# Optimization experiments

Measured on AMD Instinct MI355X. Metric: run time of the kernel, lower is better.

## Reference

```python
import jax, jax.numpy as jnp
import numpy as np

B, L = 64, 200
NQ = 1024          # n_question == output_dim
NPID = 4096
D = 256            # q_embed_dim
H = 512            # hidden_dim
Q = 1024           # output_dim
L2 = 1e-05


def setup_inputs() -> dict:
    key = jax.random.key(0)
    ks = jax.random.split(key, 20)
    q_data = jax.random.randint(ks[0], (B, L), 1, NQ + 1)          # question ids in [1, NQ]
    ans = jax.random.randint(ks[1], (B, L), 0, 2)
    qa_data = q_data + NQ * ans                                     # encoded (q, answer)
    pid_data = jax.random.randint(ks[2], (B, L), 0, NPID + 1)
    matrix = jax.random.uniform(ks[3], (Q, Q), jnp.float32) * 0.05  # p_c_relations
    u = jax.random.uniform(ks[4], (B, L))
    target = jnp.where(u < 0.1, -1.0, jnp.where(u < 0.55, 0.0, 1.0)).astype(jnp.float32)
    s = 0.05
    q_emb = jax.random.normal(ks[5], (NQ + 1, D), jnp.float32) * s
    qa_emb = jax.random.normal(ks[6], (2, D), jnp.float32) * s
    q_emb_diff = jax.random.normal(ks[7], (NQ + 1, D), jnp.float32) * s
    qa_emb_diff = jax.random.normal(ks[8], (2 * NQ + 1, D), jnp.float32) * s
    diff_parm = jax.random.normal(ks[9], (NPID + 1, 1), jnp.float32) * s
    gs = 1.0 / np.sqrt(H).astype(np.float32)
    w_ih = jax.random.uniform(ks[10], (3 * H, 2 * D), jnp.float32, -gs, gs)
    w_hh = jax.random.uniform(ks[11], (3 * H, H), jnp.float32, -gs, gs)
    b_ih = jax.random.uniform(ks[12], (3 * H,), jnp.float32, -gs, gs)
    b_hh = jax.random.uniform(ks[13], (3 * H,), jnp.float32, -gs, gs)
    fc_w = jax.random.normal(ks[14], (Q, H), jnp.float32) * 0.02
    fc_b = jnp.zeros((Q,), jnp.float32)
    return dict(q_data=q_data, qa_data=qa_data, pid_data=pid_data, matrix=matrix,
                target=target, q_emb=q_emb, qa_emb=qa_emb, q_emb_diff=q_emb_diff,
                qa_emb_diff=qa_emb_diff, diff_parm=diff_parm, w_ih=w_ih, w_hh=w_hh,
                b_ih=b_ih, b_hh=b_hh, fc_w=fc_w, fc_b=fc_b)


def _gru(x, w_ih, w_hh, b_ih, b_hh):
    # PyTorch GRU, single layer, batch_first. x: [B, L, In]
    xg = jnp.einsum('bli,gi->blg', x, w_ih) + b_ih          # [B, L, 3H]
    def step(h, xg_t):
        hg = h @ w_hh.T + b_hh
        xr, xz, xn = jnp.split(xg_t, 3, axis=-1)
        hr, hz, hn = jnp.split(hg, 3, axis=-1)
        r = jax.nn.sigmoid(xr + hr)
        z = jax.nn.sigmoid(xz + hz)
        n = jnp.tanh(xn + r * hn)
        h_new = (1.0 - z) * n + z * h
        return h_new, h_new
    h0 = jnp.zeros((x.shape[0], w_hh.shape[1]), x.dtype)
    _, hs = jax.lax.scan(step, h0, xg.transpose(1, 0, 2))
    return hs.transpose(1, 0, 2)                             # [B, L, H]


def reference(q_data, qa_data, pid_data, matrix, target, q_emb, qa_emb,
              q_emb_diff, qa_emb_diff, diff_parm, w_ih, w_hh, b_ih, b_hh,
              fc_w, fc_b):
    q_embed = q_emb[q_data]                                  # [B, L, D]
    qa = (qa_data - q_data) // NQ                            # answer in {0,1}
    qa_embed = qa_emb[qa] + q_embed
    pid_embed = diff_parm[pid_data]                          # [B, L, 1]
    q_embed2 = q_embed + pid_embed * q_emb_diff[q_data]
    qa_embed2 = qa_embed + pid_embed * qa_emb_diff[qa]
    c_reg = (pid_embed ** 2).sum() * L2

    x = jnp.concatenate([qa_embed2, q_embed2], axis=-1)      # [B, L, 2D]
    gru_out = _gru(x, w_ih, w_hh, b_ih, b_hh)
    gru_out = jnp.einsum('blh,qh->blq', gru_out, fc_w) + fc_b  # [B, L, Q]

    got = jnp.einsum('blq,kq->blk', gru_out, matrix)         # [B, L, Q]
    master = jnp.where(got >= 0.4, 1.0, got)                 # threshold-to-1 only
    # mastery of the question asked at step t: master[b, t, q-1]
    mvals = jnp.take_along_axis(master, (q_data - 1)[..., None], axis=2)[..., 0]  # [B, L]

    f32 = jnp.float32
    eq = (q_data[:, :, None] == q_data[:, None, :]).astype(f32)   # [B, t, k]
    t_idx = jnp.arange(L)
    tri_strict = (t_idx[:, None] > t_idx[None, :]).astype(f32)    # k < t
    tri_incl = (t_idx[:, None] >= t_idx[None, :]).astype(f32)     # k <= t
    mast = (mvals == 1.0).astype(f32)
    notm = (mvals == 0.0).astype(f32)
    qa1 = (qa == 1).astype(f32)
    qa0 = 1.0 - qa1
    base = eq * tri_strict                                        # [B, L, L]
    mc = jnp.einsum('btk,bk->bt', base, qa1 * mast)   # master_correct
    mi = jnp.einsum('btk,bk->bt', base, qa0 * mast)   # master_incorrect
    nmc = jnp.einsum('btk,bk->bt', base, qa0 * notm)  # no_master_correct
    aa = jnp.einsum('btk,tk->bt', eq, tri_incl)       # answered_all (>= 1)

    arB = jnp.arange(B)
    idx = q_data - 1

    def dina_step(carry, xs):
        guess, slip = carry                            # [B, Q] each
        i_t, m_t, qa_t, mc_t, mi_t, nmc_t, aa_t = xs   # [B] each
        g_upd = jnp.where(m_t == 1.0, mc_t / aa_t,
                          jnp.where(qa_t == 0, 1.0 - nmc_t / aa_t, nmc_t / aa_t))
        upd_slip = (m_t == 1.0) & (qa_t == 0)
        new_g = jnp.where(upd_slip, guess[arB, i_t], g_upd)
        new_s = jnp.where(upd_slip, mi_t / aa_t, slip[arB, i_t])
        guess = guess.at[arB, i_t].set(new_g)
        slip = slip.at[arB, i_t].set(new_s)
        p = (1.0 - new_s) * (m_t * new_g + (1.0 - new_s) * (1.0 - m_t))
        return (guess, slip), p

    init = (jnp.zeros((B, Q), f32), jnp.zeros((B, Q), f32))
    xs = (idx.T, mvals.T, qa.T, mc.T, mi.T, nmc.T, aa.T)
    _, ps = jax.lax.scan(dina_step, init, xs)          # [L, B]
    preds = ps.T.reshape(-1)                           # [B*L]

    labels = target.reshape(-1)
    mask = labels > -0.9
    preds_d = jax.lax.stop_gradient(preds)             # torch detaches via torch.tensor()
    mse_sum = (((preds_d - labels) ** 2) * mask.astype(f32)).sum()
    loss = mse_sum + c_reg
    return (loss, jax.nn.sigmoid(preds_d), mask.sum())
```

## Files before the change

kernel.cpp:

```cpp
#include <hip/hip_runtime.h>
#include <hip/hip_bf16.h>
#include <math.h>

#define BB 64
#define LL 200
#define NQ 1024
#define DD 256
#define HH 512
#define QQ 1024
#define G3 1536
#define BL 12800
#define GBLK 256

#define OFF_ACC   ((size_t)0)
#define OFF_CELLS ((size_t)16)
#define OFF_HA    ((size_t)1056)
#define OFF_AQ    (OFF_HA + 65536)
#define OFF_DQ    (OFF_AQ + 1574400)
#define OFF_BQA   (OFF_DQ + 1574400)
#define OFF_CQA   (OFF_BQA + 3072)
#define OFF_WSUM  (OFF_CQA + 3072)
#define OFF_FCWT  (OFF_WSUM + 393216)
#define OFF_M2    (OFF_FCWT + 524288)
#define OFF_MB    (OFF_M2 + 524288)
#define OFF_XG    (OFF_MB + 1024)
#define OFF_GRUT  (OFF_XG + 19660800)
#define OFF_QINT  (OFF_GRUT + 6553600)
#define OFF_QAINT (OFF_QINT + 12800)
#define OFF_PIDF  (OFF_QAINT + 12800)
#define OFF_MVAL  (OFF_PIDF + 12800)
#define OFF_MC    (OFF_MVAL + 12800)
#define OFF_MI    (OFF_MC + 12800)
#define OFF_NMC   (OFF_MI + 12800)
#define OFF_AA    (OFF_NMC + 12800)
#define OFF_PREDS (OFF_AA + 12800)

typedef float f32x4 __attribute__((ext_vector_type(4)));

__device__ __forceinline__ float wave_sum64(float v) {
    #pragma unroll
    for (int o = 32; o > 0; o >>= 1) v += __shfl_down(v, o, 64);
    return v;
}

__device__ __forceinline__ f32x4 llc_load4(const float* p) {
    f32x4 v;
    asm volatile("global_load_dwordx4 %0, %1, off sc0 sc1" : "=v"(v) : "v"(p));
    return v;
}
__device__ __forceinline__ void llc_wait2(f32x4& a, f32x4& b) {
    asm volatile("s_waitcnt vmcnt(0)" : "+v"(a), "+v"(b));
}
__device__ __forceinline__ void llc_store1(float* p, float v) {
    asm volatile("global_store_dword %0, %1, off sc0 sc1" :: "v"(p), "v"(v) : "memory");
}

__device__ __forceinline__ float quad_sum(float v) {
    float t1 = __int_as_float(__builtin_amdgcn_update_dpp(
        0, __float_as_int(v), 0xB1, 0xF, 0xF, true));
    v += t1;
    float t2 = __int_as_float(__builtin_amdgcn_update_dpp(
        0, __float_as_int(v), 0x4E, 0xF, 0xF, true));
    return v + t2;
}

__global__ __launch_bounds__(256) void prep_meta(
    const int* __restrict__ q_data, const int* __restrict__ qa_data,
    const int* __restrict__ pid_data, const float* __restrict__ diff_parm,
    int* __restrict__ qint, int* __restrict__ qaint, float* __restrict__ pidf,
    float* __restrict__ acc)
{
    int r = blockIdx.x * 256 + threadIdx.x;
    float pp = 0.f;
    if (r < BL) {
        int q = q_data[r];
        qint[r] = q;
        qaint[r] = (qa_data[r] - q) / NQ;
        float pid = diff_parm[pid_data[r]];
        pidf[r] = pid;
        pp = pid * pid;
    }
    pp = wave_sum64(pp);
    __shared__ float sm[4];
    int lane = threadIdx.x & 63, w = threadIdx.x >> 6;
    if (lane == 0) sm[w] = pp;
    __syncthreads();
    if (threadIdx.x == 0) atomicAdd(&acc[0], sm[0] + sm[1] + sm[2] + sm[3]);
}

__global__ __launch_bounds__(256) void wsum_kernel(const float* __restrict__ w_ih,
                                                   float* __restrict__ wsum)
{
    int g = blockIdx.x, d = threadIdx.x;
    wsum[(size_t)g * DD + d] = w_ih[(size_t)g * 2 * DD + d] + w_ih[(size_t)g * 2 * DD + DD + d];
}

__global__ __launch_bounds__(256) void transpose_kernel(const float* __restrict__ in,
                                                        float* __restrict__ out, int R, int C)
{
    __shared__ float tile[32][33];
    int r0 = blockIdx.y * 32, c0 = blockIdx.x * 32;
    int tx = threadIdx.x & 31, ty = threadIdx.x >> 5;
    #pragma unroll
    for (int i = 0; i < 32; i += 8) {
        int r = r0 + ty + i, c = c0 + tx;
        if (r < R && c < C) tile[ty + i][tx] = in[(size_t)r * C + c];
    }
    __syncthreads();
    #pragma unroll
    for (int i = 0; i < 32; i += 8) {
        int c = c0 + ty + i, r = r0 + tx;
        if (c < C && r < R) out[(size_t)c * R + r] = tile[tx][ty + i];
    }
}

__global__ __launch_bounds__(256) void gemm_nt_dual(
    const float* __restrict__ A0, const float* __restrict__ A1, int lda,
    const float* __restrict__ B0, const float* __restrict__ B1, int ldb0, int ldb1,
    float* __restrict__ C0, float* __restrict__ C1, int ldc,
    int M, int N, int K,
    const float* __restrict__ bias0, const float* __restrict__ bias1)
{
    const int z = blockIdx.z;
    const float* A = z ? A1 : A0;
    const float* B = z ? B1 : B0;
    float* C = z ? C1 : C0;
    const int ldb = z ? ldb1 : ldb0;
    const float* bias = z ? bias1 : bias0;

    __shared__ float As[16][65];
    __shared__ float Bs[16][65];
    const int bm = blockIdx.y * 64, bn = blockIdx.x * 64;
    const int tid = threadIdx.x;
    const int tx = tid & 15, ty = tid >> 4;
    const int mm = tid >> 4, kk = tid & 15;
    float acc[4][4] = {};
    float ar[4], br[4];
    #pragma unroll
    for (int i = 0; i < 4; ++i) {
        int m = bm + mm + 16 * i;
        ar[i] = (m < M) ? A[(size_t)m * lda + kk] : 0.f;
        int n = bn + mm + 16 * i;
        br[i] = (n < N) ? B[(size_t)n * ldb + kk] : 0.f;
    }
    for (int k0 = 0; k0 < K; k0 += 16) {
        #pragma unroll
        for (int i = 0; i < 4; ++i) { As[kk][mm + 16 * i] = ar[i]; Bs[kk][mm + 16 * i] = br[i]; }
        __syncthreads();
        int kn = k0 + 16;
        if (kn < K) {
            #pragma unroll
            for (int i = 0; i < 4; ++i) {
                int m = bm + mm + 16 * i;
                ar[i] = (m < M) ? A[(size_t)m * lda + kn + kk] : 0.f;
                int n = bn + mm + 16 * i;
                br[i] = (n < N) ? B[(size_t)n * ldb + kn + kk] : 0.f;
            }
        }
        #pragma unroll
        for (int kq = 0; kq < 16; ++kq) {
            float a[4], b[4];
            #pragma unroll
            for (int i = 0; i < 4; ++i) a[i] = As[kq][ty * 4 + i];
            #pragma unroll
            for (int j = 0; j < 4; ++j) b[j] = Bs[kq][tx * 4 + j];
            #pragma unroll
            for (int i = 0; i < 4; ++i)
                #pragma unroll
                for (int j = 0; j < 4; ++j) acc[i][j] += a[i] * b[j];
        }
        __syncthreads();
    }
    #pragma unroll
    for (int i = 0; i < 4; ++i) {
        int m = bm + ty * 4 + i;
        if (m >= M) continue;
        #pragma unroll
        for (int j = 0; j < 4; ++j) {
            int n = bn + tx * 4 + j;
            if (n >= N) continue;
            C[(size_t)m * ldc + n] = acc[i][j] + (bias ? bias[n] : 0.f);
        }
    }
}

__global__ __launch_bounds__(256) void gemm_nt_splitk(
    const float* __restrict__ Ain, int lda,
    const float* __restrict__ Bin, int ldb,
    float* __restrict__ Cp, int ldc,
    int M, int N, int K4)
{
    const int z = blockIdx.z;
    const float* A = Ain + (size_t)z * K4;
    const float* B = Bin + (size_t)z * K4;
    float* C = Cp + (size_t)z * M * ldc;

    __shared__ float As[16][65];
    __shared__ float Bs[16][65];
    const int bm = blockIdx.y * 64, bn = blockIdx.x * 64;
    const int tid = threadIdx.x;
    const int tx = tid & 15, ty = tid >> 4;
    const int mm = tid >> 4, kk = tid & 15;
    float acc[4][4] = {};
    float ar[4], br[4];
    #pragma unroll
    for (int i = 0; i < 4; ++i) {
        int m = bm + mm + 16 * i;
        ar[i] = (m < M) ? A[(size_t)m * lda + kk] : 0.f;
        int n = bn + mm + 16 * i;
        br[i] = (n < N) ? B[(size_t)n * ldb + kk] : 0.f;
    }
    for (int k0 = 0; k0 < K4; k0 += 16) {
        #pragma unroll
        for (int i = 0; i < 4; ++i) { As[kk][mm + 16 * i] = ar[i]; Bs[kk][mm + 16 * i] = br[i]; }
        __syncthreads();
        int kn = k0 + 16;
        if (kn < K4) {
            #pragma unroll
            for (int i = 0; i < 4; ++i) {
                int m = bm + mm + 16 * i;
                ar[i] = (m < M) ? A[(size_t)m * lda + kn + kk] : 0.f;
                int n = bn + mm + 16 * i;
                br[i] = (n < N) ? B[(size_t)n * ldb + kn + kk] : 0.f;
            }
        }
        #pragma unroll
        for (int kq = 0; kq < 16; ++kq) {
            float a[4], b[4];
            #pragma unroll
            for (int i = 0; i < 4; ++i) a[i] = As[kq][ty * 4 + i];
            #pragma unroll
            for (int j = 0; j < 4; ++j) b[j] = Bs[kq][tx * 4 + j];
            #pragma unroll
            for (int i = 0; i < 4; ++i)
                #pragma unroll
                for (int j = 0; j < 4; ++j) acc[i][j] += a[i] * b[j];
        }
        __syncthreads();
    }
    #pragma unroll
    for (int i = 0; i < 4; ++i) {
        int m = bm + ty * 4 + i;
        if (m >= M) continue;
        #pragma unroll
        for (int j = 0; j < 4; ++j) {
            int n = bn + tx * 4 + j;
            if (n >= N) continue;
            C[(size_t)m * ldc + n] = acc[i][j];
        }
    }
}

__global__ __launch_bounds__(256) void reduce4_kernel(const float* __restrict__ p,
                                                      float* __restrict__ o, int n)
{
    int i = blockIdx.x * 256 + threadIdx.x;
    if (i < n) o[i] = p[i] + p[n + i] + p[2 * n + i] + p[3 * n + i];
}

__global__ __launch_bounds__(256) void mb_kernel(const float* __restrict__ matrix,
                                                 const float* __restrict__ fc_b,
                                                 float* __restrict__ mb)
{
    int k = blockIdx.x;
    float s = 0.f;
    for (int q = threadIdx.x; q < QQ; q += 256) s += matrix[(size_t)k * QQ + q] * fc_b[q];
    s = wave_sum64(s);
    __shared__ float sm[4];
    int lane = threadIdx.x & 63, w = threadIdx.x >> 6;
    if (lane == 0) sm[w] = s;
    __syncthreads();
    if (threadIdx.x == 0) mb[k] = sm[0] + sm[1] + sm[2] + sm[3];
}

__global__ __launch_bounds__(512) void xgt_kernel(
    const float* __restrict__ Aq, const float* __restrict__ Bqa,
    const float* __restrict__ Cqa, const float* __restrict__ Dq,
    const int* __restrict__ qint, const int* __restrict__ qaint,
    const float* __restrict__ pidf, float* __restrict__ xgT)
{
    const int t = blockIdx.x;
    __shared__ float tile[64][129];
    __shared__ int qs[BB];
    __shared__ int qas[BB];
    __shared__ float ps[BB];
    const int tid = threadIdx.x;
    if (tid < BB) {
        qs[tid] = qint[tid * LL + t];
        qas[tid] = qaint[tid * LL + t];
        ps[tid] = pidf[tid * LL + t];
    }
    __syncthreads();
    for (int g0 = 0; g0 < G3; g0 += 128) {
        #pragma unroll
        for (int it = 0; it < 16; ++it) {
            int idx = it * 512 + tid;
            int b = idx >> 7, gg = idx & 127;
            int g = g0 + gg;
            int q = qs[b], qa = qas[b];
            float pid = ps[b];
            tile[b][gg] = Aq[(size_t)q * G3 + g] + Bqa[(size_t)qa * G3 + g]
                        + pid * (Cqa[(size_t)qa * G3 + g] + Dq[(size_t)q * G3 + g]);
        }
        __syncthreads();
        #pragma unroll
        for (int it = 0; it < 16; ++it) {
            int idx = it * 512 + tid;
            int gg = idx >> 6, b = idx & 63;
            xgT[((size_t)t * G3 + g0 + gg) * BB + b] = tile[b][gg];
        }
        __syncthreads();
    }
}

__global__ __launch_bounds__(512) void gru_persist(
    const float* __restrict__ xgT,
    const float* __restrict__ w_hh,
    const float* __restrict__ b_hh,
    float* __restrict__ hA,
    float* __restrict__ gruT2,
    unsigned int* __restrict__ cells)
{
    __shared__ float hs[8][512];
    __shared__ float part[8][3][16][8];

    const int tid = threadIdx.x;
    const int bid = blockIdx.x;
    const int bg = bid >> 5;
    const int j0 = (bid & 31) * 16;
    const int wv = tid >> 6;
    const int lane = tid & 63;
    const int g = lane >> 2;
    const int s = lane & 3;

    f32x4 ws4[3][4];
    #pragma unroll
    for (int gate = 0; gate < 3; ++gate) {
        #pragma unroll
        for (int q = 0; q < 4; ++q) {
            ws4[gate][q] = *(const f32x4*)&w_hh[(size_t)(gate * HH + j0 + g) * HH
                                                + wv * 64 + q * 16 + s * 4];
        }
    }

    const int eu = tid >> 3;
    const int eb = tid & 7;
    float bhr = 0.f, bhz = 0.f, bhn = 0.f;
    if (tid < 128) {
        bhr = b_hh[j0 + eu];
        bhz = b_hh[HH + j0 + eu];
        bhn = b_hh[2 * HH + j0 + eu];
    }

    const int b0 = lane >> 4;
    const int c0 = (lane & 15) * 4;

    int cur = 0;
    for (int t = 0; t < LL; ++t) {
        float xr = 0.f, xz = 0.f, xn = 0.f;
        if (tid < 128) {
            const float* xb = xgT + (size_t)t * G3 * BB;
            int col = bg * 8 + eb;
            xr = xb[(size_t)(j0 + eu) * BB + col];
            xz = xb[(size_t)(HH + j0 + eu) * BB + col];
            xn = xb[(size_t)(2 * HH + j0 + eu) * BB + col];
        }
        if (t && tid < 64) {
            const unsigned want = (unsigned)t;
            for (;;) {
                unsigned v = want;
                if (lane < 32)
                    v = __hip_atomic_load(&cells[(bg * 32 + lane) * 4],
                                          __ATOMIC_RELAXED, __HIP_MEMORY_SCOPE_AGENT);
                if (__all((int)(v >= want))) break;
                __builtin_amdgcn_s_sleep(2);
            }
        }
        __syncthreads();

        const float* hcur = hA + (size_t)cur * (HH * BB);
        {
            const float* p0 = hcur + (size_t)(bg * 8 + b0) * HH + wv * 64 + c0;
            f32x4 va = llc_load4(p0);
            f32x4 vb = llc_load4(p0 + 4 * HH);
            llc_wait2(va, vb);
            *(f32x4*)&hs[wv][b0 * 64 + ((c0 + 8 * b0) & 63)] = va;
            *(f32x4*)&hs[wv][(b0 + 4) * 64 + ((c0 + 8 * b0 + 32) & 63)] = vb;
        }

        float acc[3][8];
        #pragma unroll
        for (int gate = 0; gate < 3; ++gate) {
            #pragma unroll
            for (int b = 0; b < 8; ++b) acc[gate][b] = 0.f;
        }
        #pragma unroll
        for (int q = 0; q < 4; ++q) {
            const int cb = q * 16 + s * 4;
            #pragma unroll
            for (int b = 0; b < 8; ++b) {
                f32x4 h4 = *(const f32x4*)&hs[wv][b * 64 + ((cb + 8 * b) & 63)];
                #pragma unroll
                for (int gate = 0; gate < 3; ++gate) {
                    acc[gate][b] += ws4[gate][q].x * h4.x + ws4[gate][q].y * h4.y
                                  + ws4[gate][q].z * h4.z + ws4[gate][q].w * h4.w;
                }
            }
        }

        #pragma unroll
        for (int gate = 0; gate < 3; ++gate) {
            #pragma unroll
            for (int b = 0; b < 8; ++b) acc[gate][b] = quad_sum(acc[gate][b]);
        }

        if (s < 3) {
            const int rot = (2 * ((g >> 2) + s)) & 7;
            #pragma unroll
            for (int hp = 0; hp < 4; ++hp) {
                const int b = hp * 2;
                float e0 = (s == 0) ? acc[0][b]     : (s == 1) ? acc[1][b]     : acc[2][b];
                float e1 = (s == 0) ? acc[0][b + 1] : (s == 1) ? acc[1][b + 1] : acc[2][b + 1];
                const int bp = (b + rot) & 7;
                *(float2*)&part[wv][s][g][bp] = make_float2(e0, e1);
            }
        }
        __syncthreads();

        if (tid < 128) {
            const int rb = eu >> 2;
            const int bp0 = (eb + 2 * (rb + 0)) & 7;
            const int bp1 = (eb + 2 * (rb + 1)) & 7;
            const int bp2 = (eb + 2 * (rb + 2)) & 7;
            float sg0 = 0.f, sg1 = 0.f, sg2 = 0.f;
            #pragma unroll
            for (int w = 0; w < 8; ++w) {
                sg0 += part[w][0][eu][bp0];
                sg1 += part[w][1][eu][bp1];
                sg2 += part[w][2][eu][bp2];
            }
            const int ku = j0 + eu;
            float hprev = hs[ku >> 6][eb * 64 + (((ku & 63) + 8 * eb) & 63)];
            float r = 1.f / (1.f + expf(-(xr + sg0 + bhr)));
            float z = 1.f / (1.f + expf(-(xz + sg1 + bhz)));
            float n = tanhf(xn + r * (sg2 + bhn));
            float hn = (1.f - z) * n + z * hprev;
            llc_store1(hA + (size_t)(cur ^ 1) * (HH * BB) + (size_t)(bg * 8 + eb) * HH + ku, hn);
            gruT2[((size_t)t * BB + bg * 8 + eb) * HH + ku] = hn;
            asm volatile("s_waitcnt vmcnt(0)" ::: "memory");
        }
        __syncthreads();
        if (tid == 0 && t + 1 < LL)
            __hip_atomic_fetch_add(&cells[bid * 4], 1u,
                                   __ATOMIC_RELAXED, __HIP_MEMORY_SCOPE_AGENT);
        cur ^= 1;
    }
}

__global__ __launch_bounds__(256) void mval_kernel(
    const float* __restrict__ gruT2,
    const float* __restrict__ M2,
    const float* __restrict__ mb,
    const int* __restrict__ qint,
    float* __restrict__ mval)
{
    int t = blockIdx.x;
    int wave = threadIdx.x >> 6, l = threadIdx.x & 63;
    for (int ii = 0; ii < 16; ++ii) {
        int b = wave * 16 + ii;
        int q = qint[b * LL + t] - 1;
        const float4* hp = (const float4*)(gruT2 + ((size_t)t * BB + b) * HH);
        const float4* mp = (const float4*)(M2 + (size_t)q * HH);
        float4 h0 = hp[l], m0 = mp[l];
        float4 h1 = hp[64 + l], m1 = mp[64 + l];
        float acc = h0.x * m0.x + h0.y * m0.y + h0.z * m0.z + h0.w * m0.w
                  + h1.x * m1.x + h1.y * m1.y + h1.z * m1.z + h1.w * m1.w;
        acc = wave_sum64(acc);
        if (l == 0) {
            float sv = acc + mb[q];
            mval[b * LL + t] = (sv >= 0.4f) ? 1.0f : sv;
        }
    }
}

__global__ __launch_bounds__(256) void stats_kernel(
    const int* __restrict__ qint, const int* __restrict__ qaint,
    const float* __restrict__ mval,
    float* __restrict__ mc, float* __restrict__ mi,
    float* __restrict__ nmc, float* __restrict__ aa)
{
    int b = blockIdx.x, tid = threadIdx.x;
    __shared__ int qs[LL];
    __shared__ int qas[LL];
    __shared__ float mv[LL];
    if (tid < LL) {
        qs[tid] = qint[b * LL + tid];
        qas[tid] = qaint[b * LL + tid];
        mv[tid] = mval[b * LL + tid];
    }
    __syncthreads();
    int t = tid;
    if (t < LL) {
        int qt = qs[t];
        float smc = 0.f, smi = 0.f, snmc = 0.f, saa = 0.f;
        for (int k = 0; k <= t; ++k) {
            if (qs[k] == qt) {
                saa += 1.f;
                if (k < t) {
                    float mk = (mv[k] == 1.f) ? 1.f : 0.f;
                    float nk = (mv[k] == 0.f) ? 1.f : 0.f;
                    float a1 = (qas[k] == 1) ? 1.f : 0.f;
                    smc += a1 * mk;
                    smi += (1.f - a1) * mk;
                    snmc += (1.f - a1) * nk;
                }
            }
        }
        mc[b * LL + t] = smc;
        mi[b * LL + t] = smi;
        nmc[b * LL + t] = snmc;
        aa[b * LL + t] = saa;
    }
}

__global__ __launch_bounds__(256) void dina_kernel(
    const int* __restrict__ qint, const int* __restrict__ qaint,
    const float* __restrict__ mval,
    const float* __restrict__ mc, const float* __restrict__ mi,
    const float* __restrict__ nmc, const float* __restrict__ aa,
    float* __restrict__ preds)
{
    int b = blockIdx.x, tid = threadIdx.x;
    __shared__ float guess[QQ], slip[QQ];
    __shared__ float s_m[LL], s_mc[LL], s_mi[LL], s_nmc[LL], s_aa[LL];
    __shared__ int s_i[LL], s_qa[LL];
    for (int i = tid; i < QQ; i += 256) { guess[i] = 0.f; slip[i] = 0.f; }
    if (tid < LL) {
        s_m[tid] = mval[b * LL + tid];
        s_mc[tid] = mc[b * LL + tid];
        s_mi[tid] = mi[b * LL + tid];
        s_nmc[tid] = nmc[b * LL + tid];
        s_aa[tid] = aa[b * LL + tid];
        s_i[tid] = qint[b * LL + tid] - 1;
        s_qa[tid] = qaint[b * LL + tid];
    }
    __syncthreads();
    if (tid == 0) {
        for (int t = 0; t < LL; ++t) {
            int i = s_i[t];
            float m = s_m[t];
            int qa = s_qa[t];
            float aat = s_aa[t];
            float g_upd = (m == 1.f) ? s_mc[t] / aat
                          : ((qa == 0) ? 1.f - s_nmc[t] / aat : s_nmc[t] / aat);
            bool us = (m == 1.f) && (qa == 0);
            float ng = us ? guess[i] : g_upd;
            float ns = us ? s_mi[t] / aat : slip[i];
            guess[i] = ng;
            slip[i] = ns;
            preds[b * LL + t] = (1.f - ns) * (m * ng + (1.f - ns) * (1.f - m));
        }
    }
}

__global__ __launch_bounds__(256) void loss_kernel(
    const float* __restrict__ preds, const float* __restrict__ target,
    float* __restrict__ out, float* __restrict__ acc)
{
    int r = blockIdx.x * 256 + threadIdx.x;
    float lm = 0.f, lc = 0.f;
    if (r < BL) {
        float p = preds[r], lab = target[r];
        float msk = (lab > -0.9f) ? 1.f : 0.f;
        float d = p - lab;
        lm = d * d * msk;
        lc = msk;
        out[1 + r] = 1.f / (1.f + expf(-p));
    }
    lm = wave_sum64(lm);
    lc = wave_sum64(lc);
    __shared__ float sm[4], sc[4];
    int lane = threadIdx.x & 63, w = threadIdx.x >> 6;
    if (lane == 0) { sm[w] = lm; sc[w] = lc; }
    __syncthreads();
    if (threadIdx.x == 0) {
        atomicAdd(&acc[1], sm[0] + sm[1] + sm[2] + sm[3]);
        atomicAdd(&acc[2], sc[0] + sc[1] + sc[2] + sc[3]);
    }
}

__global__ void final_kernel(const float* __restrict__ acc, float* __restrict__ out)
{
    out[0] = acc[1] + acc[0] * 1e-5f;
    out[1 + BL] = acc[2];
}

extern "C" void kernel_launch(void* const* d_in, const int* in_sizes, int n_in,
                              void* d_out, int out_size, void* d_ws, size_t ws_size,
                              hipStream_t stream) {
    const int* q_data = (const int*)d_in[0];
    const int* qa_data = (const int*)d_in[1];
    const int* pid_data = (const int*)d_in[2];
    const float* matrix = (const float*)d_in[3];
    const float* target = (const float*)d_in[4];
    const float* q_emb = (const float*)d_in[5];
    const float* qa_emb = (const float*)d_in[6];
    const float* q_emb_diff = (const float*)d_in[7];
    const float* qa_emb_diff = (const float*)d_in[8];
    const float* diff_parm = (const float*)d_in[9];
    const float* w_ih = (const float*)d_in[10];
    const float* w_hh = (const float*)d_in[11];
    const float* b_ih = (const float*)d_in[12];
    const float* b_hh = (const float*)d_in[13];
    const float* fc_w = (const float*)d_in[14];
    const float* fc_b = (const float*)d_in[15];
    float* out = (float*)d_out;
    float* W = (float*)d_ws;

    float* acc = W + OFF_ACC;
    unsigned int* cells = (unsigned int*)(W + OFF_CELLS);
    float* hA = W + OFF_HA;
    float* Aq = W + OFF_AQ;
    float* Dq = W + OFF_DQ;
    float* Bqa = W + OFF_BQA;
    float* Cqa = W + OFF_CQA;
    float* wsum = W + OFF_WSUM;
    float* fcwT = W + OFF_FCWT;
    float* M2 = W + OFF_M2;
    float* mb = W + OFF_MB;
    float* xgT = W + OFF_XG;
    float* m2parts = W + OFF_XG;
    float* gruT2 = W + OFF_GRUT;
    int* qint = (int*)(W + OFF_QINT);
    int* qaint = (int*)(W + OFF_QAINT);
    float* pidf = W + OFF_PIDF;
    float* mval = W + OFF_MVAL;
    float* mc = W + OFF_MC;
    float* mi = W + OFF_MI;
    float* nmc = W + OFF_NMC;
    float* aa = W + OFF_AA;
    float* preds = W + OFF_PREDS;

    hipMemsetAsync(W, 0, (OFF_HA + 2 * HH * BB) * sizeof(float), stream);

    prep_meta<<<50, 256, 0, stream>>>(q_data, qa_data, pid_data, diff_parm,
                                      qint, qaint, pidf, acc);
    wsum_kernel<<<G3, 256, 0, stream>>>(w_ih, wsum);
    transpose_kernel<<<dim3(16, 32), 256, 0, stream>>>(fc_w, fcwT, QQ, HH);

    gemm_nt_dual<<<dim3(24, 1, 2), 256, 0, stream>>>(
        qa_emb, qa_emb_diff, DD, w_ih, w_ih, 2 * DD, 2 * DD,
        Bqa, Cqa, G3, 2, G3, DD, b_ih, nullptr);
    gemm_nt_dual<<<dim3(24, 17, 2), 256, 0, stream>>>(
        q_emb, q_emb_diff, DD, wsum, w_ih + DD, DD, 2 * DD,
        Aq, Dq, G3, NQ + 1, G3, DD, nullptr, nullptr);
    gemm_nt_splitk<<<dim3(8, 16, 4), 256, 0, stream>>>(
        matrix, QQ, fcwT, QQ, m2parts, HH, QQ, HH, QQ / 4);
    reduce4_kernel<<<2048, 256, 0, stream>>>(m2parts, M2, QQ * HH);
    mb_kernel<<<QQ, 256, 0, stream>>>(matrix, fc_b, mb);

    xgt_kernel<<<LL, 512, 0, stream>>>(Aq, Bqa, Cqa, Dq, qint, qaint, pidf, xgT);

    gru_persist<<<GBLK, 512, 0, stream>>>(xgT, w_hh, b_hh, hA, gruT2, cells);

    mval_kernel<<<LL, 256, 0, stream>>>(gruT2, M2, mb, qint, mval);
    stats_kernel<<<BB, 256, 0, stream>>>(qint, qaint, mval, mc, mi, nmc, aa);
    dina_kernel<<<BB, 256, 0, stream>>>(qint, qaint, mval, mc, mi, nmc, aa, preds);
    loss_kernel<<<50, 256, 0, stream>>>(preds, target, out, acc);
    final_kernel<<<1, 1, 0, stream>>>(acc, out);
}
```

Measured before the change: 1.160 ms.

## Repartition GRU blocks and replace atomic counters with per-group sentinel flags

The persistent GRU kernel changes its work split from 8 batches × 16 units per block to 4 batches × 32 units per block. Each block now only waits on the 16 blocks that produce its batch group, instead of 32 counters. Synchronisation moves from relaxed atomic counters to step-numbered float sentinels written with LLC-coherent stores, and the x-gate buffer is rearranged into a per-batch-group layout for contiguous reads. The hidden state and sentinels reuse the Aq region, which needs a separate memset after xgt_kernel. In exchange the kernel holds twice as many weight registers and loads smaller per-step h tiles.

```diff
diff --git a/kernel.cpp b/kernel.cpp
--- a/kernel.cpp
+++ b/kernel.cpp
@@ -11,6 +11,8 @@
 #define G3 1536
 #define BL 12800
 #define GBLK 256
+#define NBG 16
+#define NUG 16
 
 #define OFF_ACC   ((size_t)0)
 #define OFF_CELLS ((size_t)16)
@@ -43,13 +45,18 @@
     return v;
 }
 
-__device__ __forceinline__ f32x4 llc_load4(const float* p) {
+__device__ __forceinline__ f32x4 llc_load4w(const float* p) {
     f32x4 v;
-    asm volatile("global_load_dwordx4 %0, %1, off sc0 sc1" : "=v"(v) : "v"(p));
+    asm volatile("global_load_dwordx4 %0, %1, off sc0 sc1\n\ts_waitcnt vmcnt(0)"
+                 : "=&v"(v) : "v"(p));
     return v;
 }
-__device__ __forceinline__ void llc_wait2(f32x4& a, f32x4& b) {
-    asm volatile("s_waitcnt vmcnt(0)" : "+v"(a), "+v"(b));
+__device__ __forceinline__ void llc_load2s(const float* p0, const float* p1,
+                                           float& a, float& b) {
+    asm volatile("global_load_dword %0, %2, off sc0 sc1\n\t"
+                 "global_load_dword %1, %3, off sc0 sc1\n\t"
+                 "s_waitcnt vmcnt(0)"
+                 : "=&v"(a), "=&v"(b) : "v"(p0), "v"(p1));
 }
 __device__ __forceinline__ void llc_store1(float* p, float v) {
     asm volatile("global_store_dword %0, %1, off sc0 sc1" :: "v"(p), "v"(v) : "memory");
@@ -277,10 +284,10 @@
     const float* __restrict__ Aq, const float* __restrict__ Bqa,
     const float* __restrict__ Cqa, const float* __restrict__ Dq,
     const int* __restrict__ qint, const int* __restrict__ qaint,
-    const float* __restrict__ pidf, float* __restrict__ xgT)
+    const float* __restrict__ pidf, float* __restrict__ xgP)
 {
     const int t = blockIdx.x;
-    __shared__ float tile[64][129];
+    __shared__ float tile[64][136];
     __shared__ int qs[BB];
     __shared__ int qas[BB];
     __shared__ float ps[BB];
@@ -304,156 +311,157 @@
         }
         __syncthreads();
         #pragma unroll
-        for (int it = 0; it < 16; ++it) {
-            int idx = it * 512 + tid;
-            int gg = idx >> 6, b = idx & 63;
-            xgT[((size_t)t * G3 + g0 + gg) * BB + b] = tile[b][gg];
+        for (int bq = 0; bq < 16; ++bq) {
+            int gg = tid >> 2, bl = tid & 3;
+            xgP[(((size_t)bq * LL + t) * G3 + g0 + gg) * 4 + bl] = tile[bq * 4 + bl][gg];
         }
         __syncthreads();
     }
 }
 
 __global__ __launch_bounds__(512) void gru_persist(
-    const float* __restrict__ xgT,
+    const float* __restrict__ xgP,
     const float* __restrict__ w_hh,
     const float* __restrict__ b_hh,
-    float* __restrict__ hA,
-    float* __restrict__ gruT2,
-    unsigned int* __restrict__ cells)
-{
-    __shared__ float hs[8][512];
+    float* __restrict__ hU,
+    float* __restrict__ sent,
+    float* __restrict__ gruT2)
+{
+    __shared__ float hs[8][256];
     __shared__ float part[8][3][16][8];
 
     const int tid = threadIdx.x;
     const int bid = blockIdx.x;
-    const int bg = bid >> 5;
-    const int j0 = (bid & 31) * 16;
+    const int bg = bid & 15;
+    const int ug = bid >> 4;
+    const int j0 = ug * 32;
     const int wv = tid >> 6;
     const int lane = tid & 63;
     const int g = lane >> 2;
     const int s = lane & 3;
 
-    f32x4 ws4[3][4];
-    #pragma unroll
-    for (int gate = 0; gate < 3; ++gate) {
-        #pragma unroll
-        for (int q = 0; q < 4; ++q) {
-            ws4[gate][q] = *(const f32x4*)&w_hh[(size_t)(gate * HH + j0 + g) * HH
-                                                + wv * 64 + q * 16 + s * 4];
-        }
-    }
-
-    const int eu = tid >> 3;
-    const int eb = tid & 7;
+    f32x4 ws4[2][3][4];
+    #pragma unroll
+    for (int half = 0; half < 2; ++half)
+        #pragma unroll
+        for (int gate = 0; gate < 3; ++gate)
+            #pragma unroll
+            for (int q = 0; q < 4; ++q)
+                ws4[half][gate][q] = *(const f32x4*)&w_hh[
+                    (size_t)(gate * HH + j0 + half * 16 + g) * HH + wv * 64 + q * 16 + s * 4];
+
+    const int eb = tid >> 5;
+    const int eu = tid & 31;
+    const int ej = j0 + eu;
     float bhr = 0.f, bhz = 0.f, bhn = 0.f;
     if (tid < 128) {
-        bhr = b_hh[j0 + eu];
-        bhz = b_hh[HH + j0 + eu];
-        bhn = b_hh[2 * HH + j0 + eu];
-    }
-
-    const int b0 = lane >> 4;
-    const int c0 = (lane & 15) * 4;
-
-    int cur = 0;
+        bhr = b_hh[ej];
+        bhz = b_hh[HH + ej];
+        bhn = b_hh[2 * HH + ej];
+    }
+
+    const int bp = lane >> 4;
+    const int kc0 = lane & 15;
+
+    const float* myxg = xgP + (size_t)bg * LL * G3 * 4;
+    float* mysent_base = sent;
+    const int p0 = wv * 2, p1 = wv * 2 + 1;
+
     for (int t = 0; t < LL; ++t) {
         float xr = 0.f, xz = 0.f, xn = 0.f;
         if (tid < 128) {
-            const float* xb = xgT + (size_t)t * G3 * BB;
-            int col = bg * 8 + eb;
-            xr = xb[(size_t)(j0 + eu) * BB + col];
-            xz = xb[(size_t)(HH + j0 + eu) * BB + col];
-            xn = xb[(size_t)(2 * HH + j0 + eu) * BB + col];
-        }
-        if (t && tid < 64) {
-            const unsigned want = (unsigned)t;
+            const float* xb = myxg + (size_t)t * G3 * 4;
+            xr = xb[(size_t)(0 * HH + ej) * 4 + eb];
+            xz = xb[(size_t)(1 * HH + ej) * 4 + eb];
+            xn = xb[(size_t)(2 * HH + ej) * 4 + eb];
+        }
+        {
+            const float want = (float)t;
+            const float* sb = mysent_base + ((size_t)(t & 1) * 256 + bg * 16) * 4;
             for (;;) {
-                unsigned v = want;
-                if (lane < 32)
-                    v = __hip_atomic_load(&cells[(bg * 32 + lane) * 4],
-                                          __ATOMIC_RELAXED, __HIP_MEMORY_SCOPE_AGENT);
-                if (__all((int)(v >= want))) break;
-                __builtin_amdgcn_s_sleep(2);
+                float s0, s1;
+                llc_load2s(sb + p0 * 4, sb + p1 * 4, s0, s1);
+                if (__all((s0 >= want) && (s1 >= want))) break;
+                __builtin_amdgcn_s_sleep(1);
             }
         }
-        __syncthreads();
-
-        const float* hcur = hA + (size_t)cur * (HH * BB);
         {
-            const float* p0 = hcur + (size_t)(bg * 8 + b0) * HH + wv * 64 + c0;
-            f32x4 va = llc_load4(p0);
-            f32x4 vb = llc_load4(p0 + 4 * HH);
-            llc_wait2(va, vb);
-            *(f32x4*)&hs[wv][b0 * 64 + ((c0 + 8 * b0) & 63)] = va;
-            *(f32x4*)&hs[wv][(b0 + 4) * 64 + ((c0 + 8 * b0 + 32) & 63)] = vb;
-        }
-
-        float acc[3][8];
-        #pragma unroll
-        for (int gate = 0; gate < 3; ++gate) {
-            #pragma unroll
-            for (int b = 0; b < 8; ++b) acc[gate][b] = 0.f;
-        }
+            const float* hc = hU + (size_t)(t & 1) * (64 * HH)
+                            + (size_t)(bg * 4 + bp) * HH + wv * 64 + kc0 * 4;
+            f32x4 v = llc_load4w(hc);
+            *(f32x4*)&hs[wv][(kc0 * 4 + ((bp + kc0) & 3)) * 4] = v;
+        }
+
+        float acc[2][3][4] = {};
         #pragma unroll
         for (int q = 0; q < 4; ++q) {
-            const int cb = q * 16 + s * 4;
-            #pragma unroll
-            for (int b = 0; b < 8; ++b) {
-                f32x4 h4 = *(const f32x4*)&hs[wv][b * 64 + ((cb + 8 * b) & 63)];
+            const int kc = q * 4 + s;
+            #pragma unroll
+            for (int bb = 0; bb < 4; ++bb) {
+                f32x4 h4 = *(const f32x4*)&hs[wv][(kc * 4 + ((bb + kc) & 3)) * 4];
                 #pragma unroll
-                for (int gate = 0; gate < 3; ++gate) {
-                    acc[gate][b] += ws4[gate][q].x * h4.x + ws4[gate][q].y * h4.y
-                                  + ws4[gate][q].z * h4.z + ws4[gate][q].w * h4.w;
+                for (int half = 0; half < 2; ++half)
+                    #pragma unroll
+                    for (int gate = 0; gate < 3; ++gate)
+                        acc[half][gate][bb] += ws4[half][gate][q].x * h4.x
+                                             + ws4[half][gate][q].y * h4.y
+                                             + ws4[half][gate][q].z * h4.z
+                                             + ws4[half][gate][q].w * h4.w;
+            }
+        }
+        #pragma unroll
+        for (int half = 0; half < 2; ++half)
+            #pragma unroll
+            for (int gate = 0; gate < 3; ++gate)
+                #pragma unroll
+                for (int bb = 0; bb < 4; ++bb)
+                    acc[half][gate][bb] = quad_sum(acc[half][gate][bb]);
+
+        if (s < 3) {
+            const int rot = (2 * ((g >> 2) + s)) & 7;
+            #pragma unroll
+            for (int half = 0; half < 2; ++half) {
+                #pragma unroll
+                for (int pp = 0; pp < 2; ++pp) {
+                    const int i0 = half * 4 + pp * 2;
+                    float e0, e1;
+                    if (s == 0)      { e0 = acc[half][0][pp * 2]; e1 = acc[half][0][pp * 2 + 1]; }
+                    else if (s == 1) { e0 = acc[half][1][pp * 2]; e1 = acc[half][1][pp * 2 + 1]; }
+                    else             { e0 = acc[half][2][pp * 2]; e1 = acc[half][2][pp * 2 + 1]; }
+                    const int ip = (i0 + rot) & 7;
+                    *(float2*)&part[wv][s][g][ip] = make_float2(e0, e1);
                 }
             }
         }
-
-        #pragma unroll
-        for (int gate = 0; gate < 3; ++gate) {
-            #pragma unroll
-            for (int b = 0; b < 8; ++b) acc[gate][b] = quad_sum(acc[gate][b]);
-        }
-
-        if (s < 3) {
-            const int rot = (2 * ((g >> 2) + s)) & 7;
-            #pragma unroll
-            for (int hp = 0; hp < 4; ++hp) {
-                const int b = hp * 2;
-                float e0 = (s == 0) ? acc[0][b]     : (s == 1) ? acc[1][b]     : acc[2][b];
-                float e1 = (s == 0) ? acc[0][b + 1] : (s == 1) ? acc[1][b + 1] : acc[2][b + 1];
-                const int bp = (b + rot) & 7;
-                *(float2*)&part[wv][s][g][bp] = make_float2(e0, e1);
+        __syncthreads();
+
+        if (tid < 128) {
+            const int gg = eu & 15, half = eu >> 4;
+            float sg[3];
+            #pragma unroll
+            for (int gate = 0; gate < 3; ++gate) {
+                const int rotg = (2 * ((gg >> 2) + gate)) & 7;
+                const int idx = (half * 4 + eb + rotg) & 7;
+                float ss = 0.f;
+                #pragma unroll
+                for (int w = 0; w < 8; ++w) ss += part[w][gate][gg][idx];
+                sg[gate] = ss;
             }
-        }
-        __syncthreads();
-
-        if (tid < 128) {
-            const int rb = eu >> 2;
-            const int bp0 = (eb + 2 * (rb + 0)) & 7;
-            const int bp1 = (eb + 2 * (rb + 1)) & 7;
-            const int bp2 = (eb + 2 * (rb + 2)) & 7;
-            float sg0 = 0.f, sg1 = 0.f, sg2 = 0.f;
-            #pragma unroll
-            for (int w = 0; w < 8; ++w) {
-                sg0 += part[w][0][eu][bp0];
-                sg1 += part[w][1][eu][bp1];
-                sg2 += part[w][2][eu][bp2];
-            }
-            const int ku = j0 + eu;
-            float hprev = hs[ku >> 6][eb * 64 + (((ku & 63) + 8 * eb) & 63)];
-            float r = 1.f / (1.f + expf(-(xr + sg0 + bhr)));
-            float z = 1.f / (1.f + expf(-(xz + sg1 + bhz)));
-            float n = tanhf(xn + r * (sg2 + bhn));
-            float hn = (1.f - z) * n + z * hprev;
-            llc_store1(hA + (size_t)(cur ^ 1) * (HH * BB) + (size_t)(bg * 8 + eb) * HH + ku, hn);
-            gruT2[((size_t)t * BB + bg * 8 + eb) * HH + ku] = hn;
+            const int kch = (ej >> 2) & 15;
+            float hprev = hs[ej >> 6][(kch * 4 + ((eb + kch) & 3)) * 4 + (ej & 3)];
+            float rg = 1.f / (1.f + expf(-(xr + sg[0] + bhr)));
+            float zg = 1.f / (1.f + expf(-(xz + sg[1] + bhz)));
+            float ng = tanhf(xn + rg * (sg[2] + bhn));
+            float hn = (1.f - zg) * ng + zg * hprev;
+            llc_store1(hU + (size_t)((t + 1) & 1) * (64 * HH)
+                          + (size_t)(bg * 4 + eb) * HH + ej, hn);
+            gruT2[((size_t)t * BB + bg * 4 + eb) * HH + ej] = hn;
             asm volatile("s_waitcnt vmcnt(0)" ::: "memory");
         }
         __syncthreads();
         if (tid == 0 && t + 1 < LL)
-            __hip_atomic_fetch_add(&cells[bid * 4], 1u,
-                                   __ATOMIC_RELAXED, __HIP_MEMORY_SCOPE_AGENT);
-        cur ^= 1;
+            llc_store1(mysent_base + ((size_t)((t + 1) & 1) * 256 + bg * 16 + ug) * 4,
+                       (float)(t + 1));
     }
 }
 
@@ -618,8 +626,6 @@
     float* W = (float*)d_ws;
 
     float* acc = W + OFF_ACC;
-    unsigned int* cells = (unsigned int*)(W + OFF_CELLS);
-    float* hA = W + OFF_HA;
     float* Aq = W + OFF_AQ;
     float* Dq = W + OFF_DQ;
     float* Bqa = W + OFF_BQA;
@@ -628,7 +634,7 @@
     float* fcwT = W + OFF_FCWT;
     float* M2 = W + OFF_M2;
     float* mb = W + OFF_MB;
-    float* xgT = W + OFF_XG;
+    float* xgP = W + OFF_XG;
     float* m2parts = W + OFF_XG;
     float* gruT2 = W + OFF_GRUT;
     int* qint = (int*)(W + OFF_QINT);
@@ -641,7 +647,10 @@
     float* aa = W + OFF_AA;
     float* preds = W + OFF_PREDS;
 
-    hipMemsetAsync(W, 0, (OFF_HA + 2 * HH * BB) * sizeof(float), stream);
+    float* hU = W + OFF_AQ;
+    float* sent = hU + 2 * 64 * HH;
+
+    hipMemsetAsync(W, 0, 1056 * sizeof(float), stream);
 
     prep_meta<<<50, 256, 0, stream>>>(q_data, qa_data, pid_data, diff_parm,
                                       qint, qaint, pidf, acc);
@@ -659,9 +668,11 @@
     reduce4_kernel<<<2048, 256, 0, stream>>>(m2parts, M2, QQ * HH);
     mb_kernel<<<QQ, 256, 0, stream>>>(matrix, fc_b, mb);
 
-    xgt_kernel<<<LL, 512, 0, stream>>>(Aq, Bqa, Cqa, Dq, qint, qaint, pidf, xgT);
-
-    gru_persist<<<GBLK, 512, 0, stream>>>(xgT, w_hh, b_hh, hA, gruT2, cells);
+    xgt_kernel<<<LL, 512, 0, stream>>>(Aq, Bqa, Cqa, Dq, qint, qaint, pidf, xgP);
+
+    hipMemsetAsync(hU, 0, (2 * 64 * HH + 2 * 256 * 4) * sizeof(float), stream);
+
+    gru_persist<<<GBLK, 512, 0, stream>>>(xgP, w_hh, b_hh, hU, sent, gruT2);
 
     mval_kernel<<<LL, 256, 0, stream>>>(gruT2, M2, mb, qint, mval);
     stats_kernel<<<BB, 256, 0, stream>>>(qint, qaint, mval, mc, mi, nmc, aa);
```

After: 1.373 ms. 1.18x slower.

## Collapse GRU step epilogue into one wave and streamline cross-block sync

Applied to the files above, without the earlier changes.

The persistent GRU kernel now does the gate epilogue, the hidden-state publish and the cross-block spin-wait all inside wave 0, with each lane handling two batch columns. The flag is set by an atomic store of the step count instead of an atomic add. The per-step barrier count drops from three __syncthreads to two LDS-only barriers, and the gruT2 writes happen after the flag is published, taking them off the critical path. The aim is shorter per-timestep latency in the serial recurrence, at the cost of doing twice the epilogue work per lane in a single wave and a more delicate barrier ordering.

```diff
diff --git a/kernel.cpp b/kernel.cpp
--- a/kernel.cpp
+++ b/kernel.cpp
@@ -64,6 +64,13 @@
     return v + t2;
 }
 
+__device__ __forceinline__ void block_sync_lds() {
+    __builtin_amdgcn_sched_barrier(0);
+    asm volatile("s_waitcnt lgkmcnt(0)" ::: "memory");
+    __builtin_amdgcn_s_barrier();
+    __builtin_amdgcn_sched_barrier(0);
+}
+
 __global__ __launch_bounds__(256) void prep_meta(
     const int* __restrict__ q_data, const int* __restrict__ qa_data,
     const int* __restrict__ pid_data, const float* __restrict__ diff_parm,
@@ -321,13 +328,14 @@
     float* __restrict__ gruT2,
     unsigned int* __restrict__ cells)
 {
-    __shared__ float hs[8][512];
-    __shared__ float part[8][3][16][8];
+    __shared__ __align__(16) float hs[8][512];
+    __shared__ __align__(16) float part[8][3][16][8];
 
     const int tid = threadIdx.x;
     const int bid = blockIdx.x;
     const int bg = bid >> 5;
-    const int j0 = (bid & 31) * 16;
+    const int ug = bid & 31;
+    const int j0 = ug * 16;
     const int wv = tid >> 6;
     const int lane = tid & 63;
     const int g = lane >> 2;
@@ -335,51 +343,31 @@
 
     f32x4 ws4[3][4];
     #pragma unroll
-    for (int gate = 0; gate < 3; ++gate) {
-        #pragma unroll
-        for (int q = 0; q < 4; ++q) {
-            ws4[gate][q] = *(const f32x4*)&w_hh[(size_t)(gate * HH + j0 + g) * HH
-                                                + wv * 64 + q * 16 + s * 4];
-        }
-    }
-
-    const int eu = tid >> 3;
-    const int eb = tid & 7;
+    for (int gate = 0; gate < 3; ++gate)
+        #pragma unroll
+        for (int q = 0; q < 4; ++q)
+            ws4[gate][q] = *(const f32x4*)&w_hh[
+                (size_t)(gate * HH + j0 + g) * HH + wv * 64 + q * 16 + s * 4];
+
+    const int eu = lane >> 2;
+    const int e0 = lane & 3;
+    const int rb = eu >> 2;
+    const int ej = j0 + eu;
+    const int slab = ej >> 6;
+    const int kc = ej & 63;
     float bhr = 0.f, bhz = 0.f, bhn = 0.f;
-    if (tid < 128) {
-        bhr = b_hh[j0 + eu];
-        bhz = b_hh[HH + j0 + eu];
-        bhn = b_hh[2 * HH + j0 + eu];
+    if (wv == 0) {
+        bhr = b_hh[ej];
+        bhz = b_hh[HH + ej];
+        bhn = b_hh[2 * HH + ej];
     }
 
     const int b0 = lane >> 4;
     const int c0 = (lane & 15) * 4;
 
-    int cur = 0;
     for (int t = 0; t < LL; ++t) {
-        float xr = 0.f, xz = 0.f, xn = 0.f;
-        if (tid < 128) {
-            const float* xb = xgT + (size_t)t * G3 * BB;
-            int col = bg * 8 + eb;
-            xr = xb[(size_t)(j0 + eu) * BB + col];
-            xz = xb[(size_t)(HH + j0 + eu) * BB + col];
-            xn = xb[(size_t)(2 * HH + j0 + eu) * BB + col];
-        }
-        if (t && tid < 64) {
-            const unsigned want = (unsigned)t;
-            for (;;) {
-                unsigned v = want;
-                if (lane < 32)
-                    v = __hip_atomic_load(&cells[(bg * 32 + lane) * 4],
-                                          __ATOMIC_RELAXED, __HIP_MEMORY_SCOPE_AGENT);
-                if (__all((int)(v >= want))) break;
-                __builtin_amdgcn_s_sleep(2);
-            }
-        }
-        __syncthreads();
-
-        const float* hcur = hA + (size_t)cur * (HH * BB);
         {
+            const float* hcur = hA + (size_t)(t & 1) * (HH * BB);
             const float* p0 = hcur + (size_t)(bg * 8 + b0) * HH + wv * 64 + c0;
             f32x4 va = llc_load4(p0);
             f32x4 vb = llc_load4(p0 + 4 * HH);
@@ -387,13 +375,18 @@
             *(f32x4*)&hs[wv][b0 * 64 + ((c0 + 8 * b0) & 63)] = va;
             *(f32x4*)&hs[wv][(b0 + 4) * 64 + ((c0 + 8 * b0 + 32) & 63)] = vb;
         }
-
-        float acc[3][8];
-        #pragma unroll
-        for (int gate = 0; gate < 3; ++gate) {
-            #pragma unroll
-            for (int b = 0; b < 8; ++b) acc[gate][b] = 0.f;
-        }
+        float xr0 = 0.f, xz0 = 0.f, xn0 = 0.f, xr1 = 0.f, xz1 = 0.f, xn1 = 0.f;
+        if (wv == 0) {
+            const float* xb = xgT + (size_t)t * (G3 * BB) + bg * 8;
+            xr0 = xb[(size_t)ej * BB + e0];
+            xr1 = xb[(size_t)ej * BB + e0 + 4];
+            xz0 = xb[(size_t)(HH + ej) * BB + e0];
+            xz1 = xb[(size_t)(HH + ej) * BB + e0 + 4];
+            xn0 = xb[(size_t)(2 * HH + ej) * BB + e0];
+            xn1 = xb[(size_t)(2 * HH + ej) * BB + e0 + 4];
+        }
+
+        float acc[3][8] = {};
         #pragma unroll
         for (int q = 0; q < 4; ++q) {
             const int cb = q * 16 + s * 4;
@@ -401,59 +394,76 @@
             for (int b = 0; b < 8; ++b) {
                 f32x4 h4 = *(const f32x4*)&hs[wv][b * 64 + ((cb + 8 * b) & 63)];
                 #pragma unroll
-                for (int gate = 0; gate < 3; ++gate) {
+                for (int gate = 0; gate < 3; ++gate)
                     acc[gate][b] += ws4[gate][q].x * h4.x + ws4[gate][q].y * h4.y
                                   + ws4[gate][q].z * h4.z + ws4[gate][q].w * h4.w;
+            }
+        }
+        #pragma unroll
+        for (int gate = 0; gate < 3; ++gate)
+            #pragma unroll
+            for (int b = 0; b < 8; ++b)
+                acc[gate][b] = quad_sum(acc[gate][b]);
+
+        if (s < 3) {
+            const int rot = (2 * ((g >> 2) + s)) & 7;
+            #pragma unroll
+            for (int hp = 0; hp < 4; ++hp) {
+                const int b = hp * 2;
+                float e0v = (s == 0) ? acc[0][b]     : (s == 1) ? acc[1][b]     : acc[2][b];
+                float e1v = (s == 0) ? acc[0][b + 1] : (s == 1) ? acc[1][b + 1] : acc[2][b + 1];
+                const int bp = (b + rot) & 7;
+                *(float2*)&part[wv][s][g][bp] = make_float2(e0v, e1v);
+            }
+        }
+        block_sync_lds();
+
+        if (wv == 0) {
+            float hn0, hn1;
+            #pragma unroll
+            for (int pass = 0; pass < 2; ++pass) {
+                const int eb = e0 + pass * 4;
+                const int bp0 = (eb + 2 * (rb + 0)) & 7;
+                const int bp1 = (eb + 2 * (rb + 1)) & 7;
+                const int bp2 = (eb + 2 * (rb + 2)) & 7;
+                float sg0 = 0.f, sg1 = 0.f, sg2 = 0.f;
+                #pragma unroll
+                for (int w = 0; w < 8; ++w) {
+                    sg0 += part[w][0][eu][bp0];
+                    sg1 += part[w][1][eu][bp1];
+                    sg2 += part[w][2][eu][bp2];
+                }
+                float hprev = hs[slab][eb * 64 + ((kc + 8 * eb) & 63)];
+                float xr = pass ? xr1 : xr0;
+                float xz = pass ? xz1 : xz0;
+                float xn = pass ? xn1 : xn0;
+                float rg = 1.f / (1.f + expf(-(xr + sg0 + bhr)));
+                float zg = 1.f / (1.f + expf(-(xz + sg1 + bhz)));
+                float ng = tanhf(xn + rg * (sg2 + bhn));
+                float hn = (1.f - zg) * ng + zg * hprev;
+                llc_store1(hA + (size_t)((t + 1) & 1) * (HH * BB)
+                              + (size_t)(bg * 8 + eb) * HH + ej, hn);
+                if (pass == 0) hn0 = hn; else hn1 = hn;
+            }
+            asm volatile("s_waitcnt vmcnt(0)" ::: "memory");
+            if (lane == 0 && t + 1 < LL)
+                __hip_atomic_store(&cells[bid * 4], (unsigned)(t + 1),
+                                   __ATOMIC_RELAXED, __HIP_MEMORY_SCOPE_AGENT);
+            gruT2[((size_t)t * BB + bg * 8 + e0) * HH + ej] = hn0;
+            gruT2[((size_t)t * BB + bg * 8 + e0 + 4) * HH + ej] = hn1;
+            if (t + 1 < LL) {
+                const unsigned want = (unsigned)(t + 1);
+                for (;;) {
+                    unsigned v = want;
+                    if (lane < 32)
+                        v = __hip_atomic_load(&cells[(bg * 32 + lane) * 4],
+                                              __ATOMIC_RELAXED, __HIP_MEMORY_SCOPE_AGENT);
+                    if (__all((int)(v >= want))) break;
+                    __builtin_amdgcn_s_sleep(2);
                 }
             }
         }
-
-        #pragma unroll
-        for (int gate = 0; gate < 3; ++gate) {
-            #pragma unroll
-            for (int b = 0; b < 8; ++b) acc[gate][b] = quad_sum(acc[gate][b]);
-        }
-
-        if (s < 3) {
-            const int rot = (2 * ((g >> 2) + s)) & 7;
-            #pragma unroll
-            for (int hp = 0; hp < 4; ++hp) {
-                const int b = hp * 2;
-                float e0 = (s == 0) ? acc[0][b]     : (s == 1) ? acc[1][b]     : acc[2][b];
-                float e1 = (s == 0) ? acc[0][b + 1] : (s == 1) ? acc[1][b + 1] : acc[2][b + 1];
-                const int bp = (b + rot) & 7;
-                *(float2*)&part[wv][s][g][bp] = make_float2(e0, e1);
-            }
-        }
-        __syncthreads();
-
-        if (tid < 128) {
-            const int rb = eu >> 2;
-            const int bp0 = (eb + 2 * (rb + 0)) & 7;
-            const int bp1 = (eb + 2 * (rb + 1)) & 7;
-            const int bp2 = (eb + 2 * (rb + 2)) & 7;
-            float sg0 = 0.f, sg1 = 0.f, sg2 = 0.f;
-            #pragma unroll
-            for (int w = 0; w < 8; ++w) {
-                sg0 += part[w][0][eu][bp0];
-                sg1 += part[w][1][eu][bp1];
-                sg2 += part[w][2][eu][bp2];
-            }
-            const int ku = j0 + eu;
-            float hprev = hs[ku >> 6][eb * 64 + (((ku & 63) + 8 * eb) & 63)];
-            float r = 1.f / (1.f + expf(-(xr + sg0 + bhr)));
-            float z = 1.f / (1.f + expf(-(xz + sg1 + bhz)));
-            float n = tanhf(xn + r * (sg2 + bhn));
-            float hn = (1.f - z) * n + z * hprev;
-            llc_store1(hA + (size_t)(cur ^ 1) * (HH * BB) + (size_t)(bg * 8 + eb) * HH + ku, hn);
-            gruT2[((size_t)t * BB + bg * 8 + eb) * HH + ku] = hn;
-            asm volatile("s_waitcnt vmcnt(0)" ::: "memory");
-        }
-        __syncthreads();
-        if (tid == 0 && t + 1 < LL)
-            __hip_atomic_fetch_add(&cells[bid * 4], 1u,
-                                   __ATOMIC_RELAXED, __HIP_MEMORY_SCOPE_AGENT);
-        cur ^= 1;
+        block_sync_lds();
     }
 }
 
```

Result: slower. 1.397 ms (+20.4%).
